# Performance work log

Measured on AMD Instinct MI355X. Metric: run time of the kernel, lower is better.

## Reference

```python
import jax, jax.numpy as jnp
import numpy as np

IGNORE_INDEX = 255
KEEP_RATIO = 0.3
MIN_KEPT = 100000
LABEL_SMOOTHING = 0.0


def setup_inputs() -> dict:
    key = jax.random.key(0)
    k1, k2 = jax.random.split(key)
    logits = jax.random.normal(k1, (8, 19, 512, 1024), dtype=jnp.float32)
    labels = jax.random.randint(k2, (8, 512, 1024), 0, 19, dtype=jnp.int64)
    return {"logits": logits, "labels": labels}


def reference(logits, labels):
    B, C, H, W = logits.shape
    # per-pixel cross entropy (reduction='none'), flattened to [N]
    logp = jax.nn.log_softmax(logits, axis=1)                      # [B,C,H,W]
    logp_flat = logp.transpose(0, 2, 3, 1).reshape(-1, C)          # [N,C]
    lab = labels.reshape(-1)                                       # [N]
    valid = lab != IGNORE_INDEX
    safe_lab = jnp.where(valid, lab, 0)
    nll = -jnp.take_along_axis(logp_flat, safe_lab[:, None], axis=1)[:, 0]
    smooth = -jnp.mean(logp_flat, axis=1)
    loss = (1.0 - LABEL_SMOOTHING) * nll + LABEL_SMOOTHING * smooth
    # torch CE with ignore_index gives 0 loss at ignored pixels
    loss = jnp.where(valid, loss, 0.0)

    n_valid = jnp.sum(valid).astype(jnp.int32)
    n_keep = jnp.maximum((KEEP_RATIO * n_valid.astype(jnp.float32)).astype(jnp.int32),
                         jnp.minimum(MIN_KEPT, n_valid))
    n_keep = jnp.minimum(n_keep, n_valid)

    # sort valid losses descending; invalid pixels pushed to the end via -inf
    masked = jnp.where(valid, loss, -jnp.inf)
    sorted_desc = -jnp.sort(-masked)
    thr = jax.lax.stop_gradient(sorted_desc[jnp.maximum(n_keep - 1, 0)])
    thr = jnp.where(n_keep < n_valid, thr, -jnp.inf)

    keep = valid & (masked >= thr)
    cnt = jnp.sum(keep).astype(loss.dtype)
    total = jnp.sum(jnp.where(keep, loss, 0.0))
    mean_kept = total / jnp.maximum(cnt, 1.0)
    # n_valid == 0 -> 0.0 (matches logits.sum()*0.0)
    return jnp.where(n_valid == 0, jnp.sum(logits) * 0.0, mean_kept)
```

## Files before the change

### kernel.cpp

```cpp
#include <hip/hip_runtime.h>
#include <math.h>

#define IGN 255
constexpr int NC = 19;
constexpr int HWsz = 512 * 1024;
constexpr int NPIX = 8 * HWsz;

struct Ctl {
  double total;
  unsigned n_valid;
  unsigned k;
  unsigned prefix;
  unsigned cnt;
  float thr;
  unsigned pad;
};

constexpr size_t HIST_OFF = 256;
constexpr size_t LOSS_OFF = 16384;

__device__ inline unsigned flip_key(unsigned u) {
  unsigned mask = (unsigned)((int)u >> 31) | 0x80000000u;
  return u ^ mask;
}
__device__ inline float unflip_val(unsigned k) {
  unsigned u = (k & 0x80000000u) ? (k ^ 0x80000000u) : ~k;
  return __uint_as_float(u);
}

__global__ void k_init(unsigned char* ws) {
  Ctl* ctl = (Ctl*)ws;
  unsigned* hist = (unsigned*)(ws + HIST_OFF);
  int t = threadIdx.x;
  if (t == 0) {
    ctl->total = 0.0; ctl->n_valid = 0; ctl->k = 0;
    ctl->prefix = 0; ctl->cnt = 0; ctl->thr = 0.f;
  }
  for (int i = t; i < 2048; i += 256) hist[i] = 0;
}

__global__ __launch_bounds__(256) void k_loss(const float* __restrict__ logits,
                                              const int* __restrict__ labels,
                                              unsigned char* __restrict__ ws) {
  Ctl* ctl = (Ctl*)ws;
  float* loss = (float*)(ws + LOSS_OFF);
  int tid = blockIdx.x * 256 + threadIdx.x;
  int n0 = tid * 4;
  int b = n0 / HWsz;
  int hw = n0 - b * HWsz;
  const float* base = logits + (size_t)(b * NC) * HWsz + hw;

  float4 v[NC];
#pragma unroll
  for (int c = 0; c < NC; ++c)
    v[c] = *reinterpret_cast<const float4*>(base + (size_t)c * HWsz);

  float4 m = v[0];
#pragma unroll
  for (int c = 1; c < NC; ++c) {
    m.x = fmaxf(m.x, v[c].x); m.y = fmaxf(m.y, v[c].y);
    m.z = fmaxf(m.z, v[c].z); m.w = fmaxf(m.w, v[c].w);
  }
  float4 s = make_float4(0.f, 0.f, 0.f, 0.f);
#pragma unroll
  for (int c = 0; c < NC; ++c) {
    s.x += __expf(v[c].x - m.x); s.y += __expf(v[c].y - m.y);
    s.z += __expf(v[c].z - m.z); s.w += __expf(v[c].w - m.w);
  }
  float4 lse;
  lse.x = m.x + __logf(s.x); lse.y = m.y + __logf(s.y);
  lse.z = m.z + __logf(s.z); lse.w = m.w + __logf(s.w);

  int4 lab = *reinterpret_cast<const int4*>(labels + n0);
  float4 vl = make_float4(0.f, 0.f, 0.f, 0.f);
#pragma unroll
  for (int c = 0; c < NC; ++c) {
    vl.x = (lab.x == c) ? v[c].x : vl.x;
    vl.y = (lab.y == c) ? v[c].y : vl.y;
    vl.z = (lab.z == c) ? v[c].z : vl.z;
    vl.w = (lab.w == c) ? v[c].w : vl.w;
  }
  float4 out;
  unsigned cnt = 0;
  out.x = (lab.x == IGN) ? -INFINITY : (lse.x - vl.x); cnt += (lab.x != IGN);
  out.y = (lab.y == IGN) ? -INFINITY : (lse.y - vl.y); cnt += (lab.y != IGN);
  out.z = (lab.z == IGN) ? -INFINITY : (lse.z - vl.z); cnt += (lab.z != IGN);
  out.w = (lab.w == IGN) ? -INFINITY : (lse.w - vl.w); cnt += (lab.w != IGN);
  *reinterpret_cast<float4*>(loss + n0) = out;

  __shared__ unsigned red[256];
  red[threadIdx.x] = cnt;
  __syncthreads();
  for (int s2 = 128; s2 > 0; s2 >>= 1) {
    if (threadIdx.x < s2) red[threadIdx.x] += red[threadIdx.x + s2];
    __syncthreads();
  }
  if (threadIdx.x == 0 && red[0]) atomicAdd(&ctl->n_valid, red[0]);
}

template <int PASS>
__global__ __launch_bounds__(256) void k_hist(unsigned char* __restrict__ ws) {
  const unsigned* keys = (const unsigned*)(ws + LOSS_OFF);
  unsigned* hist = (unsigned*)(ws + HIST_OFF);
  const Ctl* ctl = (const Ctl*)ws;
  __shared__ unsigned lh[2048];
  for (int i = threadIdx.x; i < 2048; i += 256) lh[i] = 0;
  unsigned prefix = ctl->prefix;
  __syncthreads();

  unsigned idx0 = blockIdx.x * 512 + threadIdx.x;
#pragma unroll
  for (int i = 0; i < 2; ++i) {
    uint4 u = reinterpret_cast<const uint4*>(keys)[idx0 + i * 256];
    unsigned a[4] = {u.x, u.y, u.z, u.w};
#pragma unroll
    for (int j = 0; j < 4; ++j) {
      unsigned key = flip_key(a[j]);
      if (PASS == 0) {
        atomicAdd(&lh[key >> 21], 1u);
      } else if (PASS == 1) {
        if ((key >> 21) == prefix) atomicAdd(&lh[(key >> 10) & 0x7FFu], 1u);
      } else {
        if ((key >> 10) == prefix) atomicAdd(&lh[key & 0x3FFu], 1u);
      }
    }
  }
  __syncthreads();
  for (int i = threadIdx.x; i < 2048; i += 256)
    if (lh[i]) atomicAdd(&hist[i], lh[i]);
}

template <int PASS>
__global__ __launch_bounds__(256) void k_scan(unsigned char* __restrict__ ws) {
  constexpr int NB = (PASS == 2) ? 1024 : 2048;
  constexpr int BPT = NB / 256;
  Ctl* ctl = (Ctl*)ws;
  unsigned* hist = (unsigned*)(ws + HIST_OFF);
  int t = threadIdx.x;

  unsigned k;
  if (PASS == 0) {
    unsigned nv = ctl->n_valid;
    int nk = (int)(0.3f * (float)nv);
    int mk = (100000 < (int)nv) ? 100000 : (int)nv;
    if (nk < mk) nk = mk;
    if (nk > (int)nv) nk = (int)nv;
    k = (unsigned)nk;
  } else {
    k = ctl->k;
  }

  unsigned local[BPT];
  unsigned lsum = 0;
#pragma unroll
  for (int j = 0; j < BPT; ++j) {
    unsigned v = hist[t * BPT + j];
    hist[t * BPT + j] = 0;
    local[j] = v;
    lsum += v;
  }
  __shared__ unsigned ts[256];
  ts[t] = lsum;
  __syncthreads();
  for (int off = 1; off < 256; off <<= 1) {
    unsigned add = (t + off < 256) ? ts[t + off] : 0u;
    __syncthreads();
    ts[t] += add;
    __syncthreads();
  }
  unsigned above = ts[t] - lsum;
  if (k > 0) {
#pragma unroll
    for (int j = BPT - 1; j >= 0; --j) {
      unsigned cbin = local[j];
      unsigned tot = above + cbin;
      if (above < k && tot >= k) {
        unsigned bin = (unsigned)(t * BPT + j);
        unsigned kk = k - above;
        if (PASS == 0) {
          ctl->prefix = bin; ctl->k = kk;
        } else if (PASS == 1) {
          ctl->prefix = (ctl->prefix << 11) | bin; ctl->k = kk;
        } else {
          unsigned key = (ctl->prefix << 10) | bin;
          ctl->thr = unflip_val(key);
        }
      }
      above = tot;
    }
  }
}

__global__ __launch_bounds__(256) void k_final(unsigned char* __restrict__ ws) {
  const float* loss = (const float*)(ws + LOSS_OFF);
  Ctl* ctl = (Ctl*)ws;
  float thr = ctl->thr;
  unsigned idx0 = blockIdx.x * 512 + threadIdx.x;
  float s = 0.f;
  unsigned c = 0;
#pragma unroll
  for (int i = 0; i < 2; ++i) {
    float4 v = reinterpret_cast<const float4*>(loss)[idx0 + i * 256];
    if (v.x >= thr) { s += v.x; c++; }
    if (v.y >= thr) { s += v.y; c++; }
    if (v.z >= thr) { s += v.z; c++; }
    if (v.w >= thr) { s += v.w; c++; }
  }
  double sd = (double)s;
  for (int off = 32; off > 0; off >>= 1) {
    sd += __shfl_down(sd, off);
    c += __shfl_down(c, off);
  }
  __shared__ double sred[4];
  __shared__ unsigned cred[4];
  int wave = threadIdx.x >> 6, lane = threadIdx.x & 63;
  if (lane == 0) { sred[wave] = sd; cred[wave] = c; }
  __syncthreads();
  if (threadIdx.x == 0) {
    double st = sred[0] + sred[1] + sred[2] + sred[3];
    unsigned ct = cred[0] + cred[1] + cred[2] + cred[3];
    atomicAdd(&ctl->total, st);
    atomicAdd(&ctl->cnt, ct);
  }
}

__global__ void k_fin(unsigned char* __restrict__ ws, float* __restrict__ out) {
  if (threadIdx.x == 0) {
    Ctl* ctl = (Ctl*)ws;
    float r = 0.f;
    if (ctl->n_valid != 0) {
      unsigned c = ctl->cnt; if (c < 1u) c = 1u;
      r = (float)(ctl->total / (double)c);
    }
    out[0] = r;
  }
}

extern "C" void kernel_launch(void* const* d_in, const int* in_sizes, int n_in,
                              void* d_out, int out_size, void* d_ws, size_t ws_size,
                              hipStream_t stream) {
  const float* logits = (const float*)d_in[0];
  const int* labels = (const int*)d_in[1];
  float* out = (float*)d_out;
  unsigned char* ws = (unsigned char*)d_ws;

  hipLaunchKernelGGL(k_init, dim3(1), dim3(256), 0, stream, ws);
  hipLaunchKernelGGL(k_loss, dim3(NPIX / 4 / 256), dim3(256), 0, stream, logits, labels, ws);
  hipLaunchKernelGGL((k_hist<0>), dim3(NPIX / 8 / 256), dim3(256), 0, stream, ws);
  hipLaunchKernelGGL((k_scan<0>), dim3(1), dim3(256), 0, stream, ws);
  hipLaunchKernelGGL((k_hist<1>), dim3(NPIX / 8 / 256), dim3(256), 0, stream, ws);
  hipLaunchKernelGGL((k_scan<1>), dim3(1), dim3(256), 0, stream, ws);
  hipLaunchKernelGGL((k_hist<2>), dim3(NPIX / 8 / 256), dim3(256), 0, stream, ws);
  hipLaunchKernelGGL((k_scan<2>), dim3(1), dim3(256), 0, stream, ws);
  hipLaunchKernelGGL(k_final, dim3(NPIX / 8 / 256), dim3(256), 0, stream, ws);
  hipLaunchKernelGGL(k_fin, dim3(1), dim3(64), 0, stream, ws, out);
}
```

Before: 215.5 us.

## Fuse first histogram into loss kernel and recompute scans per block

```diff
diff --git a/kernel.cpp b/kernel.cpp
--- a/kernel.cpp
+++ b/kernel.cpp
@@ -6,18 +6,19 @@
 constexpr int HWsz = 512 * 1024;
 constexpr int NPIX = 8 * HWsz;
 
+typedef float v4f __attribute__((ext_vector_type(4)));
+typedef int v4i __attribute__((ext_vector_type(4)));
+typedef unsigned v4u __attribute__((ext_vector_type(4)));
+
 struct Ctl {
   double total;
-  unsigned n_valid;
-  unsigned k;
-  unsigned prefix;
-  unsigned cnt;
-  float thr;
-  unsigned pad;
+  unsigned n_valid, cnt, done, pad;
 };
 
-constexpr size_t HIST_OFF = 256;
-constexpr size_t LOSS_OFF = 16384;
+constexpr size_t H0 = 256;
+constexpr size_t H1 = H0 + 2048 * 4;
+constexpr size_t H2 = H1 + 2048 * 4;
+constexpr size_t LOSS_OFF = 65536;
 
 __device__ inline unsigned flip_key(unsigned u) {
   unsigned mask = (unsigned)((int)u >> 31) | 0x80000000u;
@@ -27,139 +28,25 @@
   unsigned u = (k & 0x80000000u) ? (k ^ 0x80000000u) : ~k;
   return __uint_as_float(u);
 }
-
-__global__ void k_init(unsigned char* ws) {
-  Ctl* ctl = (Ctl*)ws;
-  unsigned* hist = (unsigned*)(ws + HIST_OFF);
+__device__ inline unsigned compute_k(unsigned nv) {
+  int nk = (int)(0.3f * (float)nv);
+  int mk = (100000 < (int)nv) ? 100000 : (int)nv;
+  if (nk < mk) nk = mk;
+  if (nk > (int)nv) nk = (int)nv;
+  return (unsigned)nk;
+}
+
+template <int NB>
+__device__ inline void selscan(const unsigned* __restrict__ hist, unsigned k,
+                               unsigned& bin, unsigned& kk) {
+  constexpr int BPT = NB / 256;
+  __shared__ unsigned ts[256];
+  __shared__ unsigned bb[2];
   int t = threadIdx.x;
-  if (t == 0) {
-    ctl->total = 0.0; ctl->n_valid = 0; ctl->k = 0;
-    ctl->prefix = 0; ctl->cnt = 0; ctl->thr = 0.f;
-  }
-  for (int i = t; i < 2048; i += 256) hist[i] = 0;
-}
-
-__global__ __launch_bounds__(256) void k_loss(const float* __restrict__ logits,
-                                              const int* __restrict__ labels,
-                                              unsigned char* __restrict__ ws) {
-  Ctl* ctl = (Ctl*)ws;
-  float* loss = (float*)(ws + LOSS_OFF);
-  int tid = blockIdx.x * 256 + threadIdx.x;
-  int n0 = tid * 4;
-  int b = n0 / HWsz;
-  int hw = n0 - b * HWsz;
-  const float* base = logits + (size_t)(b * NC) * HWsz + hw;
-
-  float4 v[NC];
-#pragma unroll
-  for (int c = 0; c < NC; ++c)
-    v[c] = *reinterpret_cast<const float4*>(base + (size_t)c * HWsz);
-
-  float4 m = v[0];
-#pragma unroll
-  for (int c = 1; c < NC; ++c) {
-    m.x = fmaxf(m.x, v[c].x); m.y = fmaxf(m.y, v[c].y);
-    m.z = fmaxf(m.z, v[c].z); m.w = fmaxf(m.w, v[c].w);
-  }
-  float4 s = make_float4(0.f, 0.f, 0.f, 0.f);
-#pragma unroll
-  for (int c = 0; c < NC; ++c) {
-    s.x += __expf(v[c].x - m.x); s.y += __expf(v[c].y - m.y);
-    s.z += __expf(v[c].z - m.z); s.w += __expf(v[c].w - m.w);
-  }
-  float4 lse;
-  lse.x = m.x + __logf(s.x); lse.y = m.y + __logf(s.y);
-  lse.z = m.z + __logf(s.z); lse.w = m.w + __logf(s.w);
-
-  int4 lab = *reinterpret_cast<const int4*>(labels + n0);
-  float4 vl = make_float4(0.f, 0.f, 0.f, 0.f);
-#pragma unroll
-  for (int c = 0; c < NC; ++c) {
-    vl.x = (lab.x == c) ? v[c].x : vl.x;
-    vl.y = (lab.y == c) ? v[c].y : vl.y;
-    vl.z = (lab.z == c) ? v[c].z : vl.z;
-    vl.w = (lab.w == c) ? v[c].w : vl.w;
-  }
-  float4 out;
-  unsigned cnt = 0;
-  out.x = (lab.x == IGN) ? -INFINITY : (lse.x - vl.x); cnt += (lab.x != IGN);
-  out.y = (lab.y == IGN) ? -INFINITY : (lse.y - vl.y); cnt += (lab.y != IGN);
-  out.z = (lab.z == IGN) ? -INFINITY : (lse.z - vl.z); cnt += (lab.z != IGN);
-  out.w = (lab.w == IGN) ? -INFINITY : (lse.w - vl.w); cnt += (lab.w != IGN);
-  *reinterpret_cast<float4*>(loss + n0) = out;
-
-  __shared__ unsigned red[256];
-  red[threadIdx.x] = cnt;
-  __syncthreads();
-  for (int s2 = 128; s2 > 0; s2 >>= 1) {
-    if (threadIdx.x < s2) red[threadIdx.x] += red[threadIdx.x + s2];
-    __syncthreads();
-  }
-  if (threadIdx.x == 0 && red[0]) atomicAdd(&ctl->n_valid, red[0]);
-}
-
-template <int PASS>
-__global__ __launch_bounds__(256) void k_hist(unsigned char* __restrict__ ws) {
-  const unsigned* keys = (const unsigned*)(ws + LOSS_OFF);
-  unsigned* hist = (unsigned*)(ws + HIST_OFF);
-  const Ctl* ctl = (const Ctl*)ws;
-  __shared__ unsigned lh[2048];
-  for (int i = threadIdx.x; i < 2048; i += 256) lh[i] = 0;
-  unsigned prefix = ctl->prefix;
-  __syncthreads();
-
-  unsigned idx0 = blockIdx.x * 512 + threadIdx.x;
-#pragma unroll
-  for (int i = 0; i < 2; ++i) {
-    uint4 u = reinterpret_cast<const uint4*>(keys)[idx0 + i * 256];
-    unsigned a[4] = {u.x, u.y, u.z, u.w};
-#pragma unroll
-    for (int j = 0; j < 4; ++j) {
-      unsigned key = flip_key(a[j]);
-      if (PASS == 0) {
-        atomicAdd(&lh[key >> 21], 1u);
-      } else if (PASS == 1) {
-        if ((key >> 21) == prefix) atomicAdd(&lh[(key >> 10) & 0x7FFu], 1u);
-      } else {
-        if ((key >> 10) == prefix) atomicAdd(&lh[key & 0x3FFu], 1u);
-      }
-    }
-  }
-  __syncthreads();
-  for (int i = threadIdx.x; i < 2048; i += 256)
-    if (lh[i]) atomicAdd(&hist[i], lh[i]);
-}
-
-template <int PASS>
-__global__ __launch_bounds__(256) void k_scan(unsigned char* __restrict__ ws) {
-  constexpr int NB = (PASS == 2) ? 1024 : 2048;
-  constexpr int BPT = NB / 256;
-  Ctl* ctl = (Ctl*)ws;
-  unsigned* hist = (unsigned*)(ws + HIST_OFF);
-  int t = threadIdx.x;
-
-  unsigned k;
-  if (PASS == 0) {
-    unsigned nv = ctl->n_valid;
-    int nk = (int)(0.3f * (float)nv);
-    int mk = (100000 < (int)nv) ? 100000 : (int)nv;
-    if (nk < mk) nk = mk;
-    if (nk > (int)nv) nk = (int)nv;
-    k = (unsigned)nk;
-  } else {
-    k = ctl->k;
-  }
-
   unsigned local[BPT];
   unsigned lsum = 0;
 #pragma unroll
-  for (int j = 0; j < BPT; ++j) {
-    unsigned v = hist[t * BPT + j];
-    hist[t * BPT + j] = 0;
-    local[j] = v;
-    lsum += v;
-  }
-  __shared__ unsigned ts[256];
+  for (int j = 0; j < BPT; ++j) { local[j] = hist[t * BPT + j]; lsum += local[j]; }
   ts[t] = lsum;
   __syncthreads();
   for (int off = 1; off < 256; off <<= 1) {
@@ -169,42 +56,184 @@
     __syncthreads();
   }
   unsigned above = ts[t] - lsum;
+  if (t == 0) { bb[0] = 0xFFFFFFFFu; bb[1] = 0u; }
+  __syncthreads();
   if (k > 0) {
 #pragma unroll
     for (int j = BPT - 1; j >= 0; --j) {
-      unsigned cbin = local[j];
-      unsigned tot = above + cbin;
-      if (above < k && tot >= k) {
-        unsigned bin = (unsigned)(t * BPT + j);
-        unsigned kk = k - above;
-        if (PASS == 0) {
-          ctl->prefix = bin; ctl->k = kk;
-        } else if (PASS == 1) {
-          ctl->prefix = (ctl->prefix << 11) | bin; ctl->k = kk;
-        } else {
-          unsigned key = (ctl->prefix << 10) | bin;
-          ctl->thr = unflip_val(key);
-        }
-      }
+      unsigned cb = local[j];
+      unsigned tot = above + cb;
+      if (above < k && tot >= k) { bb[0] = (unsigned)(t * BPT + j); bb[1] = k - above; }
       above = tot;
     }
   }
-}
-
-__global__ __launch_bounds__(256) void k_final(unsigned char* __restrict__ ws) {
+  __syncthreads();
+  bin = bb[0];
+  kk = bb[1];
+  __syncthreads();
+}
+
+__global__ void k_init(unsigned char* ws) {
+  Ctl* ctl = (Ctl*)ws;
+  unsigned* h = (unsigned*)(ws + H0);
+  int t = threadIdx.x;
+  if (t == 0) { ctl->total = 0.0; ctl->n_valid = 0; ctl->cnt = 0; ctl->done = 0; }
+  for (int i = t; i < 5120; i += 256) h[i] = 0;
+}
+
+__global__ __launch_bounds__(256) void k_loss(const float* __restrict__ logits,
+                                              const int* __restrict__ labels,
+                                              unsigned char* __restrict__ ws) {
+  Ctl* ctl = (Ctl*)ws;
+  float* loss = (float*)(ws + LOSS_OFF);
+  unsigned* h0 = (unsigned*)(ws + H0);
+  __shared__ unsigned lh[2048];
+  __shared__ unsigned red[256];
+  for (int i = threadIdx.x; i < 2048; i += 256) lh[i] = 0;
+  __syncthreads();
+
+  int tid = blockIdx.x * 256 + threadIdx.x;
+  int n0 = tid * 4;
+  int b = n0 >> 19;
+  int hw = n0 & (HWsz - 1);
+  const float* base = logits + (size_t)(b * NC) * HWsz + hw;
+
+  v4f v[NC];
+#pragma unroll
+  for (int c = 0; c < NC; ++c)
+    v[c] = __builtin_nontemporal_load(reinterpret_cast<const v4f*>(base + (size_t)c * HWsz));
+
+  v4f m = v[0];
+#pragma unroll
+  for (int c = 1; c < NC; ++c) {
+    m[0] = fmaxf(m[0], v[c][0]); m[1] = fmaxf(m[1], v[c][1]);
+    m[2] = fmaxf(m[2], v[c][2]); m[3] = fmaxf(m[3], v[c][3]);
+  }
+  v4f s = (v4f)(0.f);
+#pragma unroll
+  for (int c = 0; c < NC; ++c) {
+    s[0] += __expf(v[c][0] - m[0]); s[1] += __expf(v[c][1] - m[1]);
+    s[2] += __expf(v[c][2] - m[2]); s[3] += __expf(v[c][3] - m[3]);
+  }
+  v4f lse;
+  lse[0] = m[0] + __logf(s[0]); lse[1] = m[1] + __logf(s[1]);
+  lse[2] = m[2] + __logf(s[2]); lse[3] = m[3] + __logf(s[3]);
+
+  v4i lab = *reinterpret_cast<const v4i*>(labels + n0);
+  v4f vl = (v4f)(0.f);
+#pragma unroll
+  for (int c = 0; c < NC; ++c) {
+    vl[0] = (lab[0] == c) ? v[c][0] : vl[0];
+    vl[1] = (lab[1] == c) ? v[c][1] : vl[1];
+    vl[2] = (lab[2] == c) ? v[c][2] : vl[2];
+    vl[3] = (lab[3] == c) ? v[c][3] : vl[3];
+  }
+  v4f out;
+  unsigned cnt = 0;
+  out[0] = (lab[0] == IGN) ? -INFINITY : (lse[0] - vl[0]); cnt += (lab[0] != IGN);
+  out[1] = (lab[1] == IGN) ? -INFINITY : (lse[1] - vl[1]); cnt += (lab[1] != IGN);
+  out[2] = (lab[2] == IGN) ? -INFINITY : (lse[2] - vl[2]); cnt += (lab[2] != IGN);
+  out[3] = (lab[3] == IGN) ? -INFINITY : (lse[3] - vl[3]); cnt += (lab[3] != IGN);
+  *reinterpret_cast<v4f*>(loss + n0) = out;
+
+  atomicAdd(&lh[flip_key(__float_as_uint(out[0])) >> 21], 1u);
+  atomicAdd(&lh[flip_key(__float_as_uint(out[1])) >> 21], 1u);
+  atomicAdd(&lh[flip_key(__float_as_uint(out[2])) >> 21], 1u);
+  atomicAdd(&lh[flip_key(__float_as_uint(out[3])) >> 21], 1u);
+
+  red[threadIdx.x] = cnt;
+  __syncthreads();
+  for (int s2 = 128; s2 > 0; s2 >>= 1) {
+    if (threadIdx.x < s2) red[threadIdx.x] += red[threadIdx.x + s2];
+    __syncthreads();
+  }
+  if (threadIdx.x == 0 && red[0]) atomicAdd(&ctl->n_valid, red[0]);
+  for (int i = threadIdx.x; i < 2048; i += 256)
+    if (lh[i]) atomicAdd(&h0[i], lh[i]);
+}
+
+__global__ __launch_bounds__(256) void k_hist1(unsigned char* __restrict__ ws) {
+  Ctl* ctl = (Ctl*)ws;
+  const unsigned* keys = (const unsigned*)(ws + LOSS_OFF);
+  unsigned* h0 = (unsigned*)(ws + H0);
+  unsigned* h1 = (unsigned*)(ws + H1);
+  __shared__ unsigned lh[2048];
+  unsigned k0 = compute_k(ctl->n_valid);
+  unsigned p0, k1;
+  selscan<2048>(h0, k0, p0, k1);
+  for (int i = threadIdx.x; i < 2048; i += 256) lh[i] = 0;
+  __syncthreads();
+
+  unsigned idx0 = blockIdx.x * 512 + threadIdx.x;
+#pragma unroll
+  for (int i = 0; i < 2; ++i) {
+    v4u u = reinterpret_cast<const v4u*>(keys)[idx0 + i * 256];
+#pragma unroll
+    for (int j = 0; j < 4; ++j) {
+      unsigned key = flip_key(u[j]);
+      if ((key >> 21) == p0) atomicAdd(&lh[(key >> 10) & 0x7FFu], 1u);
+    }
+  }
+  __syncthreads();
+  for (int i = threadIdx.x; i < 2048; i += 256)
+    if (lh[i]) atomicAdd(&h1[i], lh[i]);
+}
+
+__global__ __launch_bounds__(256) void k_hist2(unsigned char* __restrict__ ws) {
+  Ctl* ctl = (Ctl*)ws;
+  const unsigned* keys = (const unsigned*)(ws + LOSS_OFF);
+  unsigned* h0 = (unsigned*)(ws + H0);
+  unsigned* h1 = (unsigned*)(ws + H1);
+  unsigned* h2 = (unsigned*)(ws + H2);
+  __shared__ unsigned lh[1024];
+  unsigned k0 = compute_k(ctl->n_valid);
+  unsigned p0, k1, p1, k2;
+  selscan<2048>(h0, k0, p0, k1);
+  selscan<2048>(h1, k1, p1, k2);
+  unsigned pp = (p0 << 11) | p1;
+  for (int i = threadIdx.x; i < 1024; i += 256) lh[i] = 0;
+  __syncthreads();
+
+  unsigned idx0 = blockIdx.x * 512 + threadIdx.x;
+#pragma unroll
+  for (int i = 0; i < 2; ++i) {
+    v4u u = reinterpret_cast<const v4u*>(keys)[idx0 + i * 256];
+#pragma unroll
+    for (int j = 0; j < 4; ++j) {
+      unsigned key = flip_key(u[j]);
+      if ((key >> 10) == pp) atomicAdd(&lh[key & 0x3FFu], 1u);
+    }
+  }
+  __syncthreads();
+  for (int i = threadIdx.x; i < 1024; i += 256)
+    if (lh[i]) atomicAdd(&h2[i], lh[i]);
+}
+
+__global__ __launch_bounds__(256) void k_final(unsigned char* __restrict__ ws,
+                                               float* __restrict__ out) {
+  Ctl* ctl = (Ctl*)ws;
   const float* loss = (const float*)(ws + LOSS_OFF);
-  Ctl* ctl = (Ctl*)ws;
-  float thr = ctl->thr;
+  unsigned* h0 = (unsigned*)(ws + H0);
+  unsigned* h1 = (unsigned*)(ws + H1);
+  unsigned* h2 = (unsigned*)(ws + H2);
+  unsigned k0 = compute_k(ctl->n_valid);
+  unsigned p0, k1, p1, k2, b2, kf;
+  selscan<2048>(h0, k0, p0, k1);
+  selscan<2048>(h1, k1, p1, k2);
+  selscan<1024>(h2, k2, b2, kf);
+  float thr = INFINITY;
+  if (k0 > 0) thr = unflip_val((((p0 << 11) | p1) << 10) | b2);
+
   unsigned idx0 = blockIdx.x * 512 + threadIdx.x;
   float s = 0.f;
   unsigned c = 0;
 #pragma unroll
   for (int i = 0; i < 2; ++i) {
-    float4 v = reinterpret_cast<const float4*>(loss)[idx0 + i * 256];
-    if (v.x >= thr) { s += v.x; c++; }
-    if (v.y >= thr) { s += v.y; c++; }
-    if (v.z >= thr) { s += v.z; c++; }
-    if (v.w >= thr) { s += v.w; c++; }
+    v4f v = reinterpret_cast<const v4f*>(loss)[idx0 + i * 256];
+    if (v[0] >= thr) { s += v[0]; c++; }
+    if (v[1] >= thr) { s += v[1]; c++; }
+    if (v[2] >= thr) { s += v[2]; c++; }
+    if (v[3] >= thr) { s += v[3]; c++; }
   }
   double sd = (double)s;
   for (int off = 32; off > 0; off >>= 1) {
@@ -221,18 +250,18 @@
     unsigned ct = cred[0] + cred[1] + cred[2] + cred[3];
     atomicAdd(&ctl->total, st);
     atomicAdd(&ctl->cnt, ct);
-  }
-}
-
-__global__ void k_fin(unsigned char* __restrict__ ws, float* __restrict__ out) {
-  if (threadIdx.x == 0) {
-    Ctl* ctl = (Ctl*)ws;
-    float r = 0.f;
-    if (ctl->n_valid != 0) {
-      unsigned c = ctl->cnt; if (c < 1u) c = 1u;
-      r = (float)(ctl->total / (double)c);
-    }
-    out[0] = r;
+    __threadfence();
+    unsigned prev = atomicAdd(&ctl->done, 1u);
+    if (prev == gridDim.x - 1) {
+      double tt = atomicAdd(&ctl->total, 0.0);
+      unsigned cc = atomicAdd(&ctl->cnt, 0u);
+      float r = 0.f;
+      if (ctl->n_valid != 0) {
+        if (cc < 1u) cc = 1u;
+        r = (float)(tt / (double)cc);
+      }
+      out[0] = r;
+    }
   }
 }
 
@@ -246,12 +275,7 @@
 
   hipLaunchKernelGGL(k_init, dim3(1), dim3(256), 0, stream, ws);
   hipLaunchKernelGGL(k_loss, dim3(NPIX / 4 / 256), dim3(256), 0, stream, logits, labels, ws);
-  hipLaunchKernelGGL((k_hist<0>), dim3(NPIX / 8 / 256), dim3(256), 0, stream, ws);
-  hipLaunchKernelGGL((k_scan<0>), dim3(1), dim3(256), 0, stream, ws);
-  hipLaunchKernelGGL((k_hist<1>), dim3(NPIX / 8 / 256), dim3(256), 0, stream, ws);
-  hipLaunchKernelGGL((k_scan<1>), dim3(1), dim3(256), 0, stream, ws);
-  hipLaunchKernelGGL((k_hist<2>), dim3(NPIX / 8 / 256), dim3(256), 0, stream, ws);
-  hipLaunchKernelGGL((k_scan<2>), dim3(1), dim3(256), 0, stream, ws);
-  hipLaunchKernelGGL(k_final, dim3(NPIX / 8 / 256), dim3(256), 0, stream, ws);
-  hipLaunchKernelGGL(k_fin, dim3(1), dim3(64), 0, stream, ws, out);
-}
+  hipLaunchKernelGGL(k_hist1, dim3(NPIX / 8 / 256), dim3(256), 0, stream, ws);
+  hipLaunchKernelGGL(k_hist2, dim3(NPIX / 8 / 256), dim3(256), 0, stream, ws);
+  hipLaunchKernelGGL(k_final, dim3(NPIX / 8 / 256), dim3(256), 0, stream, ws, out);
+}
```

Measured after the change: 215.1 us. Within noise of the previous version (-0.2%).
